# Kernel optimization log

Hardware: AMD Instinct MI355X
Metric: run time of the kernel (lower is better)

## Reference

```python
import jax, jax.numpy as jnp
import numpy as np

B, S, D = 1, 4096, 1024
H, KVH, HD = 16, 4, 64  # heads, kv heads, head_dim; GQA groups = H//KVH
EOS_PROB = 0.05


def rotate_half(x):
    h = x.shape[-1] // 2
    return jnp.concatenate([-x[..., h:], x[..., :h]], axis=-1)


def setup_inputs() -> dict:
    key = jax.random.key(0)
    ks = jax.random.split(key, 8)
    hidden_states = jax.random.normal(ks[0], (B, S, D), jnp.float32) * 0.02
    # standard RoPE tables, [B, S, HD]
    inv_freq = 1.0 / (10000.0 ** (jnp.arange(0, HD, 2, dtype=jnp.float32) / HD))
    freqs = jnp.outer(jnp.arange(S, dtype=jnp.float32), inv_freq)
    emb = jnp.concatenate([freqs, freqs], axis=-1)
    cos = jnp.broadcast_to(jnp.cos(emb)[None], (B, S, HD))
    sin = jnp.broadcast_to(jnp.sin(emb)[None], (B, S, HD))
    sc = D ** -0.5
    Wq = jax.random.normal(ks[1], (D, H * HD), jnp.float32) * sc
    Wk = jax.random.normal(ks[2], (D, KVH * HD), jnp.float32) * sc
    Wv = jax.random.normal(ks[3], (D, KVH * HD), jnp.float32) * sc
    Wo = jax.random.normal(ks[4], (H * HD, D), jnp.float32) * sc
    # sentence-boundary (end-of-sentence / special) token mask, ~1 EOS per 20 tokens
    special = (jax.random.uniform(ks[5], (B, S)) < EOS_PROB).astype(jnp.int32)
    special = special.at[:, 0].set(1)  # BOS acts as a boundary token
    # closest end-of-sentence token index at or before each position
    pos = jnp.arange(S, dtype=jnp.int32)
    marked = jnp.where(special.astype(bool), pos[None, :], jnp.int32(-1))
    eos_idx = jax.lax.associative_scan(jnp.maximum, marked, axis=1)
    eos_idx = jnp.maximum(eos_idx, 0).astype(jnp.int32)
    return {
        'hidden_states': hidden_states, 'cos': cos, 'sin': sin,
        'Wq': Wq, 'Wk': Wk, 'Wv': Wv, 'Wo': Wo,
        'special_embeddings_mask': special,
        'clothest_end_of_sentence_token_idx': eos_idx,
    }


def reference(hidden_states, cos, sin, Wq, Wk, Wv, Wo,
              special_embeddings_mask, clothest_end_of_sentence_token_idx):
    b, s, d = hidden_states.shape
    # projections -> [b, h, s, hd]
    q = (hidden_states @ Wq).reshape(b, s, H, HD).transpose(0, 2, 1, 3)
    k = (hidden_states @ Wk).reshape(b, s, KVH, HD).transpose(0, 2, 1, 3)
    v = (hidden_states @ Wv).reshape(b, s, KVH, HD).transpose(0, 2, 1, 3)
    # RoPE
    c = cos[:, None, :, :]
    sn = sin[:, None, :, :]
    q = q * c + rotate_half(q) * sn
    k = k * c + rotate_half(k) * sn
    # GQA: repeat kv heads
    groups = H // KVH
    k = jnp.repeat(k, groups, axis=1)
    v = jnp.repeat(v, groups, axis=1)
    scores = jnp.einsum('bhqd,bhkd->bhqk', q, k) * (HD ** -0.5)
    # sentence-structured mask: causal AND (key inside current sentence OR key is
    # an end-of-sentence/special boundary token)
    pos = jnp.arange(s, dtype=jnp.int32)
    causal = (pos[None, :] <= pos[:, None])[None, None]           # [1,1,s,s]
    special_k = special_embeddings_mask.astype(bool)[:, None, None, :]  # [b,1,1,s]
    eos = clothest_end_of_sentence_token_idx[:, None, :, None]    # [b,1,s,1]
    allowed = causal & ((pos[None, None, None, :] >= eos) | special_k)
    scores = jnp.where(allowed, scores, jnp.asarray(-1e9, scores.dtype))
    probs = jax.nn.softmax(scores, axis=-1)
    attn = jnp.einsum('bhqk,bhkd->bhqd', probs, v)
    attn = attn.transpose(0, 2, 1, 3).reshape(b, s, H * HD)
    return attn @ Wo
```

## Files before the change

### kernel.cpp

```cpp
#include <hip/hip_runtime.h>

typedef __bf16 bf16x8 __attribute__((ext_vector_type(8)));
typedef float f32x4 __attribute__((ext_vector_type(4)));
typedef short s16x8 __attribute__((ext_vector_type(8)));
typedef short s16x4 __attribute__((ext_vector_type(4)));
typedef unsigned short u16;
typedef unsigned int u32;
typedef unsigned long long u64;

#define S_LEN 4096
#define DMODEL 1024
#define NH 16
#define HD 64

static __device__ __forceinline__ u16 f2bf(float f) {
  union { float f; u32 u; } a; a.f = f;
  u32 r = (a.u + 0x7fffu + ((a.u >> 16) & 1u)) >> 16;
  return (u16)r;
}

static __device__ __forceinline__ f32x4 mfma16(bf16x8 a, bf16x8 b, f32x4 c) {
  return __builtin_amdgcn_mfma_f32_16x16x32_bf16(a, b, c, 0, 0, 0);
}

static __device__ __forceinline__ f32x4 mfma16x16(s16x4 a, s16x4 b, f32x4 c) {
#if __has_builtin(__builtin_amdgcn_mfma_f32_16x16x16bf16_1k)
  return __builtin_amdgcn_mfma_f32_16x16x16bf16_1k(a, b, c, 0, 0, 0);
#else
  asm("v_mfma_f32_16x16x16_bf16 %0, %1, %2, %0" : "+v"(c) : "v"(a), "v"(b));
  return c;
#endif
}

static __device__ __forceinline__ void gload16(const void* g, void* l) {
  __builtin_amdgcn_global_load_lds((const __attribute__((address_space(1))) u32*)g,
                                   (__attribute__((address_space(3))) u32*)l, 16, 0, 0);
}

static __device__ __forceinline__ int xcd_swz(int id, int nwg) {
  return (id & 7) * (nwg >> 3) + (id >> 3);
}

__global__ __launch_bounds__(256)
void prep_kernel(const float* __restrict__ hidden, const float* __restrict__ Wq,
                 const float* __restrict__ Wk, const float* __restrict__ Wv,
                 const float* __restrict__ Wo, const int* __restrict__ spec,
                 const int* __restrict__ eosi,
                 u16* __restrict__ hbf, u16* __restrict__ wqkvT, u16* __restrict__ woT,
                 u64* __restrict__ spb, int* __restrict__ sidx, int* __restrict__ scnt,
                 int4* __restrict__ qmeta) {
  __shared__ float ftile[32][33];
  __shared__ u64 smask[64];
  __shared__ int scnt_s[64];
  __shared__ int spref[64];

  const int bx = (int)blockIdx.x;
  const int t = (int)threadIdx.x;

  if (bx < 4096) {
    const int i = (bx * 256 + t) * 4;
    const float4 v = *(const float4*)(hidden + i);
    uint2 o;
    o.x = (u32)f2bf(v.x) | ((u32)f2bf(v.y) << 16);
    o.y = (u32)f2bf(v.z) | ((u32)f2bf(v.w) << 16);
    *(uint2*)(hbf + i) = o;
    return;
  }
  if (bx < 6656) {
    const float* W; u16* WT; int N, loc, nbx;
    if (bx < 5120)      { W = Wq; WT = wqkvT;               N = 1024; loc = bx - 4096; nbx = 32; }
    else if (bx < 5376) { W = Wk; WT = wqkvT + 1024 * 1024; N = 256;  loc = bx - 5120; nbx = 8; }
    else if (bx < 5632) { W = Wv; WT = wqkvT + 1280 * 1024; N = 256;  loc = bx - 5376; nbx = 8; }
    else                { W = Wo; WT = woT;                 N = 1024; loc = bx - 5632; nbx = 32; }
    const int n0 = (loc % nbx) * 32, k0 = (loc / nbx) * 32;
    const int tx = t & 31, ty = t >> 5;
#pragma unroll
    for (int i = 0; i < 4; ++i)
      ftile[ty + 8 * i][tx] = W[(size_t)(k0 + ty + 8 * i) * N + n0 + tx];
    __syncthreads();
#pragma unroll
    for (int i = 0; i < 4; ++i)
      WT[(size_t)(n0 + ty + 8 * i) * 1024 + k0 + tx] = f2bf(ftile[tx][ty + 8 * i]);
    return;
  }
  const int wv = t >> 6, l = t & 63;
#pragma unroll
  for (int i = 0; i < 16; ++i) {
    const int b = wv * 16 + i;
    const u64 m = __ballot(spec[b * 64 + l] != 0);
    if (l == 0) { smask[b] = m; scnt_s[b] = __popcll(m); }
  }
  __syncthreads();
  if (wv == 0) {
    const int v = scnt_s[l];
    int inc = v;
#pragma unroll
    for (int d = 1; d < 64; d <<= 1) {
      const int o = __shfl_up(inc, d);
      if (l >= d) inc += o;
    }
    spref[l] = inc - v;
    if (l == 63) scnt[0] = inc;
    spb[l] = smask[l];
  }
  __syncthreads();
#pragma unroll
  for (int i = 0; i < 16; ++i) {
    const int b = wv * 16 + i;
    const u64 m = smask[b];
    if ((m >> l) & 1ull)
      sidx[spref[b] + __popcll(m & ((1ull << l) - 1ull))] = b * 64 + l;
  }
  if (t < 64) {
    const int e = eosi[t * 64];
    const int tlo = e >> 6;
    const int nsp = spref[tlo];
    const int nspt = (nsp + 63) >> 6;
    qmeta[t] = make_int4(tlo, nspt, nspt + (t - tlo + 1), nsp);
  }
}

__global__ __launch_bounds__(256)
void pack_kernel(const u16* __restrict__ Kb, const u16* __restrict__ Vtg,
                 const int* __restrict__ sidx, const int* __restrict__ scnt,
                 u16* __restrict__ Kg, u16* __restrict__ Vgt) {
  __shared__ int rowidx[64];
  const int nspec = scnt[0];
  const int j0 = (int)blockIdx.x * 64;
  if (j0 >= nspec) return;
  const int kvh = (int)blockIdx.y;
  const int t = (int)threadIdx.x;
  if (t < 64) rowidx[t] = (j0 + t < nspec) ? sidx[j0 + t] : 0;
  __syncthreads();
  {
    const int r = t >> 2;
    const int s = rowidx[r];
    const int j = j0 + r;
    const u16* srcrow = Kb + (size_t)s * 256 + kvh * 64;
    u16* dstrow = Kg + (size_t)j * 256 + kvh * 64;
    const int x = (j ^ s) & 7;
#pragma unroll
    for (int a = 0; a < 2; ++a) {
      const int cd = (t & 3) * 2 + a;
      *(s16x8*)(dstrow + cd * 8) = *(const s16x8*)(srcrow + ((cd ^ x) * 8));
    }
  }
  {
    const int d = t >> 2;
    const u16* srcrow = Vtg + (size_t)(kvh * 64 + d) * 4096;
    u16* drow = Vgt + (size_t)(kvh * 64 + d) * 4096 + j0;
    const int xd = (d & 7) << 3;
#pragma unroll
    for (int a = 0; a < 2; ++a) {
      const int jc = (t & 3) * 2 + a;
      s16x8 o;
#pragma unroll
      for (int e = 0; e < 8; ++e) {
        const int s = rowidx[jc * 8 + e];
        o[e] = (short)srcrow[(s & ~63) + ((s & 63) ^ xd)];
      }
      *(s16x8*)(drow + ((jc * 8) ^ xd)) = o;
    }
  }
}

template <int MODE>
__global__ __launch_bounds__(256, 3)
void gemm128(const u16* __restrict__ A, const u16* __restrict__ BT,
             const float* __restrict__ cosp, const float* __restrict__ sinp,
             u16* __restrict__ Qb, u16* __restrict__ Kb, u16* __restrict__ Vtg,
             float* __restrict__ Cf) {
  __shared__ __align__(16) u16 As[128 * 32];
  __shared__ __align__(16) u16 Bs[64 * 32];
  const int t = (int)threadIdx.x;
  const int w = t >> 6;
  const int lane = t & 63;
  const int lr = lane & 15, lg = lane >> 4;

  const int nx = (int)gridDim.x;
  const int nwg = nx * (int)gridDim.y;
  const int id = xcd_swz((int)blockIdx.x + (int)blockIdx.y * nx, nwg);
  const int m0 = (id / nx) * 128;
  const int n0 = (id % nx) * 64;
  const int wm = w * 32;

  f32x4 acc[2][4] = {};

  const int srow = t >> 2;
  const int scol = (t & 3) * 8;

  for (int k0 = 0; k0 < 1024; k0 += 32) {
    gload16(A + (size_t)(m0 + srow) * 1024 + k0 + scol, As + t * 8);
    gload16(A + (size_t)(m0 + 64 + srow) * 1024 + k0 + scol, As + 2048 + t * 8);
    gload16(BT + (size_t)(n0 + srow) * 1024 + k0 + scol, Bs + t * 8);
    __syncthreads();
    bf16x8 af[2], bg[4];
#pragma unroll
    for (int mi = 0; mi < 2; ++mi)
      af[mi] = *(const bf16x8*)(As + (wm + mi * 16 + lr) * 32 + lg * 8);
#pragma unroll
    for (int ni = 0; ni < 4; ++ni)
      bg[ni] = *(const bf16x8*)(Bs + (ni * 16 + lr) * 32 + lg * 8);
#pragma unroll
    for (int mi = 0; mi < 2; ++mi)
#pragma unroll
      for (int ni = 0; ni < 4; ++ni)
        acc[mi][ni] = mfma16(af[mi], bg[ni], acc[mi][ni]);
    __syncthreads();
  }

  if (MODE == 0) {
#pragma unroll
    for (int mi = 0; mi < 2; ++mi)
#pragma unroll
      for (int r = 0; r < 4; ++r) {
        const int m = m0 + wm + mi * 16 + lg * 4 + r;
#pragma unroll
        for (int ni = 0; ni < 4; ++ni)
          Cf[(size_t)m * 1024 + n0 + ni * 16 + lr] = acc[mi][ni][r];
      }
  } else if (n0 < 1280) {
#pragma unroll
    for (int mi = 0; mi < 2; ++mi)
#pragma unroll
      for (int r = 0; r < 4; ++r) {
        const int m = m0 + wm + mi * 16 + lg * 4 + r;
        const float* cr = cosp + (size_t)m * 64;
        const float* sr = sinp + (size_t)m * 64;
        float o[4];
#pragma unroll
        for (int ni = 0; ni < 2; ++ni) {
          const int d1 = ni * 16 + lr, d2 = d1 + 32;
          const float x = acc[mi][ni][r], y = acc[mi][ni + 2][r];
          o[ni]     = x * cr[d1] - y * sr[d1];
          o[ni + 2] = y * cr[d2] + x * sr[d2];
        }
        if (n0 < 1024) {
          u16* dst = Qb + (size_t)m * 1024 + n0;
#pragma unroll
          for (int ni = 0; ni < 4; ++ni) dst[ni * 16 + lr] = f2bf(o[ni]);
        } else {
          u16* dst = Kb + (size_t)m * 256 + (n0 - 1024);
          const int sw = (m & 7) << 3;
#pragma unroll
          for (int ni = 0; ni < 4; ++ni) dst[(ni * 16 + lr) ^ sw] = f2bf(o[ni]);
        }
      }
  } else {
    const int kvh = (n0 - 1280) >> 6;
#pragma unroll
    for (int ni = 0; ni < 4; ++ni) {
      const int d = ni * 16 + lr;
      u16* vrow = Vtg + (size_t)(kvh * 64 + d) * 4096;
      const int xd = (d & 7) << 3;
#pragma unroll
      for (int mi = 0; mi < 2; ++mi) {
        const int sb = m0 + wm + mi * 16 + lg * 4;
        const int os = (sb & ~63) | ((sb & 63) ^ xd);
        uint2 pkv;
        pkv.x = (u32)f2bf(acc[mi][ni][0]) | ((u32)f2bf(acc[mi][ni][1]) << 16);
        pkv.y = (u32)f2bf(acc[mi][ni][2]) | ((u32)f2bf(acc[mi][ni][3]) << 16);
        *(uint2*)(vrow + os) = pkv;
      }
    }
  }
}

__global__ __launch_bounds__(256, 5)
void attn_kernel(const u16* __restrict__ Qb, const u16* __restrict__ Kb,
                 const u16* __restrict__ Vtg, const u16* __restrict__ Kg,
                 const u16* __restrict__ Vgt, const u64* __restrict__ spb,
                 const int* __restrict__ eosi, const int4* __restrict__ qmeta,
                 u16* __restrict__ Ob) {
  __shared__ __align__(16) u16 lds[2][2][4096];

  const int id = xcd_swz((int)blockIdx.x + (int)blockIdx.y * 64, 1024);
  const int qt = 63 - (id & 63);
  const int h = id >> 6;
  const int kvh = h >> 2;
  const int t = (int)threadIdx.x;
  const int w = t >> 6;
  const int lane = t & 63;
  const int lr = lane & 15, lg = lane >> 4;
  const int q0 = qt * 64;
  const int q = q0 + w * 16 + lr;
  const int swl = (lr & 7) << 3;

  const int4 qm = qmeta[qt];
  const int tile_lo = qm.x;
  const int nit = qm.z;
  const int nsp = qm.w;
  const int nloc = qt - tile_lo + 1;

  bf16x8 aq[2];
  {
    const u16* qp = Qb + (size_t)q * 1024 + h * 64 + lg * 8;
    aq[0] = *(const bf16x8*)qp;
    aq[1] = *(const bf16x8*)(qp + 32);
  }
  const int eos_q = eosi[q];

  f32x4 acc[4] = {};
  float mrow = -3.0e38f;
  float lrow = 0.0f;

  const int grow = t >> 3;
  const int gcol = (t & 7) * 8;

  auto STAGE = [&](int buf, int it) {
    const u16 *kp, *vp;
    if (it < nloc) {
      const int kbase = (tile_lo + it) * 64;
      kp = Kb + (size_t)kbase * 256 + kvh * 64;
      vp = Vtg + (size_t)(kvh * 64) * 4096 + kbase;
    } else {
      const int jb = (it - nloc) * 64;
      kp = Kg + (size_t)jb * 256 + kvh * 64;
      vp = Vgt + (size_t)(kvh * 64) * 4096 + jb;
    }
#pragma unroll
    for (int i = 0; i < 2; ++i) {
      gload16(kp + (size_t)(i * 32 + grow) * 256 + gcol, &lds[buf][0][i * 2048 + t * 8]);
      gload16(vp + (size_t)(i * 32 + grow) * 4096 + gcol, &lds[buf][1][i * 2048 + t * 8]);
    }
  };

  STAGE(0, 0);
  __syncthreads();

  for (int it = 0; it < nit; ++it) {
    if (it + 1 < nit) STAGE((it + 1) & 1, it + 1);
    const u16* Kl = &lds[it & 1][0][0];
    const u16* Vl = &lds[it & 1][1][0];

    f32x4 st[4];
#pragma unroll
    for (int kt = 0; kt < 4; ++kt) {
      f32x4 s = {};
#pragma unroll
      for (int c = 0; c < 2; ++c) {
        bf16x8 ak = *(const bf16x8*)(Kl + (kt * 16 + lr) * 64 + ((c * 32 + lg * 8) ^ swl));
        s = mfma16(ak, aq[c], s);
      }
      st[kt] = s;
    }

    u64 allowed;
    if (it < nloc) {
      const int kbase = (tile_lo + it) * 64;
      const u64 spec = spb[tile_lo + it];
      const int dq = q - kbase;
      const u64 causal = (dq >= 63) ? ~0ull : ((2ull << dq) - 1ull);
      const int de = eos_q - kbase;
      const u64 ge = (de <= 0) ? ~0ull : (de >= 64 ? 0ull : (~0ull << de));
      allowed = causal & (ge | spec);
    } else {
      const int rem = nsp - (it - nloc) * 64;
      allowed = (rem >= 64) ? ~0ull : ((1ull << rem) - 1ull);
    }

    float xs[16];
    float tmax = -3.0e38f;
#pragma unroll
    for (int kt = 0; kt < 4; ++kt) {
      const u32 bits = (u32)(allowed >> (kt * 16 + lg * 4)) & 0xFu;
#pragma unroll
      for (int r = 0; r < 4; ++r) {
        const float x = ((bits >> r) & 1u) ? st[kt][r] * 0.18033688011112042f : -3.0e38f;
        xs[kt * 4 + r] = x;
        tmax = fmaxf(tmax, x);
      }
    }
    tmax = fmaxf(tmax, __shfl_xor(tmax, 16));
    tmax = fmaxf(tmax, __shfl_xor(tmax, 32));
    const float mn = fmaxf(mrow, tmax);
    const float resc = exp2f(mrow - mn);
    mrow = mn;

    float rs = 0.0f;
    u32 pk[8];
#pragma unroll
    for (int i = 0; i < 16; i += 2) {
      const float p0 = exp2f(xs[i] - mn);
      const float p1 = exp2f(xs[i + 1] - mn);
      rs += p0 + p1;
      pk[i >> 1] = (u32)f2bf(p0) | ((u32)f2bf(p1) << 16);
    }
    rs += __shfl_xor(rs, 16);
    rs += __shfl_xor(rs, 32);
    lrow = lrow * resc + rs;

#pragma unroll
    for (int dt = 0; dt < 4; ++dt)
#pragma unroll
      for (int r = 0; r < 4; ++r) acc[dt][r] *= resc;

#pragma unroll
    for (int kt = 0; kt < 4; ++kt) {
      union { u32 u[2]; s16x4 v; } cv;
      cv.u[0] = pk[kt * 2]; cv.u[1] = pk[kt * 2 + 1];
      const int vo = (kt * 16 + lg * 4) ^ swl;
#pragma unroll
      for (int dt = 0; dt < 4; ++dt) {
        s16x4 av = *(const s16x4*)(Vl + (dt * 16 + lr) * 64 + vo);
        acc[dt] = mfma16x16(av, cv.v, acc[dt]);
      }
    }
    __syncthreads();
  }

  const float inv = 1.0f / lrow;
#pragma unroll
  for (int dt = 0; dt < 4; ++dt) {
    const u32 w0 = (u32)f2bf(acc[dt][0] * inv) | ((u32)f2bf(acc[dt][1] * inv) << 16);
    const u32 w1 = (u32)f2bf(acc[dt][2] * inv) | ((u32)f2bf(acc[dt][3] * inv) << 16);
    u32* dst = (u32*)(Ob + (size_t)q * 1024 + h * 64 + dt * 16 + lg * 4);
    dst[0] = w0; dst[1] = w1;
  }
}

extern "C" void kernel_launch(void* const* d_in, const int* in_sizes, int n_in,
                              void* d_out, int out_size, void* d_ws, size_t ws_size,
                              hipStream_t stream) {
  (void)in_sizes; (void)n_in; (void)out_size; (void)ws_size;
  const float* hidden = (const float*)d_in[0];
  const float* cosp   = (const float*)d_in[1];
  const float* sinp   = (const float*)d_in[2];
  const float* Wq     = (const float*)d_in[3];
  const float* Wk     = (const float*)d_in[4];
  const float* Wv     = (const float*)d_in[5];
  const float* Wo     = (const float*)d_in[6];
  const int* spec     = (const int*)d_in[7];
  const int* eosi     = (const int*)d_in[8];
  float* out = (float*)d_out;

  u16* ws = (u16*)d_ws;
  u16* hbf   = ws;
  u16* wqkvT = hbf + 4194304;
  u16* woT   = wqkvT + 1572864;
  u16* Qb    = woT + 1048576;
  u16* Kb    = Qb + 4194304;
  u16* Vtg   = Kb + 1048576;
  u16* Ob    = Vtg + 1048576;
  u16* tail  = Ob + 4194304;
  u64* spb   = (u64*)tail;
  int* sidx  = (int*)(tail + 256);
  int* scnt  = (int*)(tail + 8448);
  int4* qmeta = (int4*)(tail + 8512);
  u16* Kg    = hbf;
  u16* Vgt   = hbf + 1048576;

  prep_kernel<<<dim3(6657), dim3(256), 0, stream>>>(hidden, Wq, Wk, Wv, Wo, spec, eosi,
                                                    hbf, wqkvT, woT, spb, sidx, scnt, qmeta);
  gemm128<1><<<dim3(24, 32), dim3(256), 0, stream>>>(hbf, wqkvT, cosp, sinp,
                                                     Qb, Kb, Vtg, nullptr);
  pack_kernel<<<dim3(64, 4), dim3(256), 0, stream>>>(Kb, Vtg, sidx, scnt, Kg, Vgt);
  attn_kernel<<<dim3(64, 16), dim3(256), 0, stream>>>(Qb, Kb, Vtg, Kg, Vgt, spb,
                                                      eosi, qmeta, Ob);
  gemm128<0><<<dim3(16, 32), dim3(256), 0, stream>>>(Ob, woT, nullptr, nullptr,
                                                     nullptr, nullptr, nullptr, out);
}
```

Measured before the change: 90.07 us.

## Double-buffer GEMM LDS tiles with BK=64 and XOR-swizzled layout

Rewrites the projection GEMM main loop to use two LDS buffers with a K-tile of 64, prefetching the next tile while computing the current one, and halving the number of barriers. The LDS layout is XOR-swizzled by row to avoid bank conflicts on the 16-byte fragment reads. This increases LDS use to 48KB per block, which may reduce occupancy relative to the launch_bounds target of 3 blocks per CU.

```diff
diff --git a/kernel.cpp b/kernel.cpp
--- a/kernel.cpp
+++ b/kernel.cpp
@@ -170,8 +170,8 @@
              const float* __restrict__ cosp, const float* __restrict__ sinp,
              u16* __restrict__ Qb, u16* __restrict__ Kb, u16* __restrict__ Vtg,
              float* __restrict__ Cf) {
-  __shared__ __align__(16) u16 As[128 * 32];
-  __shared__ __align__(16) u16 Bs[64 * 32];
+  __shared__ __align__(16) u16 As[2][128 * 64];
+  __shared__ __align__(16) u16 Bs[2][64 * 64];
   const int t = (int)threadIdx.x;
   const int w = t >> 6;
   const int lane = t & 63;
@@ -186,26 +186,49 @@
 
   f32x4 acc[2][4] = {};
 
-  const int srow = t >> 2;
-  const int scol = (t & 3) * 8;
-
-  for (int k0 = 0; k0 < 1024; k0 += 32) {
-    gload16(A + (size_t)(m0 + srow) * 1024 + k0 + scol, As + t * 8);
-    gload16(A + (size_t)(m0 + 64 + srow) * 1024 + k0 + scol, As + 2048 + t * 8);
-    gload16(BT + (size_t)(n0 + srow) * 1024 + k0 + scol, Bs + t * 8);
-    __syncthreads();
-    bf16x8 af[2], bg[4];
-#pragma unroll
-    for (int mi = 0; mi < 2; ++mi)
-      af[mi] = *(const bf16x8*)(As + (wm + mi * 16 + lr) * 32 + lg * 8);
-#pragma unroll
-    for (int ni = 0; ni < 4; ++ni)
-      bg[ni] = *(const bf16x8*)(Bs + (ni * 16 + lr) * 32 + lg * 8);
-#pragma unroll
-    for (int mi = 0; mi < 2; ++mi)
-#pragma unroll
-      for (int ni = 0; ni < 4; ++ni)
-        acc[mi][ni] = mfma16(af[mi], bg[ni], acc[mi][ni]);
+  const int srow = t >> 3;
+  const int sp = t & 7;
+
+  auto STAGE = [&](int buf, int k0) {
+#pragma unroll
+    for (int i = 0; i < 4; ++i) {
+      const int j = i * 32 + srow;
+      gload16(A + (size_t)(m0 + j) * 1024 + k0 + ((sp ^ (j & 7)) * 8),
+              &As[buf][i * 2048 + t * 8]);
+    }
+#pragma unroll
+    for (int i = 0; i < 2; ++i) {
+      const int j = i * 32 + srow;
+      gload16(BT + (size_t)(n0 + j) * 1024 + k0 + ((sp ^ (j & 7)) * 8),
+              &Bs[buf][i * 2048 + t * 8]);
+    }
+  };
+
+  STAGE(0, 0);
+  __syncthreads();
+
+  for (int it = 0; it < 16; ++it) {
+    const int cur = it & 1;
+    if (it + 1 < 16) STAGE(cur ^ 1, (it + 1) * 64);
+#pragma unroll
+    for (int c = 0; c < 2; ++c) {
+      bf16x8 af[2], bg[4];
+#pragma unroll
+      for (int mi = 0; mi < 2; ++mi) {
+        const int row = wm + mi * 16 + lr;
+        af[mi] = *(const bf16x8*)&As[cur][row * 64 + (((c * 4 + lg) ^ (row & 7)) * 8)];
+      }
+#pragma unroll
+      for (int ni = 0; ni < 4; ++ni) {
+        const int row = ni * 16 + lr;
+        bg[ni] = *(const bf16x8*)&Bs[cur][row * 64 + (((c * 4 + lg) ^ (row & 7)) * 8)];
+      }
+#pragma unroll
+      for (int mi = 0; mi < 2; ++mi)
+#pragma unroll
+        for (int ni = 0; ni < 4; ++ni)
+          acc[mi][ni] = mfma16(af[mi], bg[ni], acc[mi][ni]);
+    }
     __syncthreads();
   }
 
```

Result: faster. 82.03 us (-8.9%).
